# Kernel optimization log

Measured on AMD Instinct MI355X. Metric: run time of the kernel, lower is better.

The kernel has to match this reference:

```python
import jax, jax.numpy as jnp
import numpy as np

B, D, H, T = 256, 1024, 1024, 100
EPS = 1e-5  # torch LayerNorm default

def _ln(x, g, b):
    m = jnp.mean(x, axis=-1, keepdims=True)
    v = jnp.mean((x - m) ** 2, axis=-1, keepdims=True)
    return (x - m) * jax.lax.rsqrt(v + EPS) * g + b

def _gru_cell(x, h, Wih, Whh, bih, bhh):
    # PyTorch GRUCell math. Wih:[3H,in], Whh:[3H,H], gate order r,z,n.
    gi = x @ Wih.T + bih
    gh = h @ Whh.T + bhh
    ir, iz, inn = jnp.split(gi, 3, axis=-1)
    hr, hz, hn = jnp.split(gh, 3, axis=-1)
    r = jax.nn.sigmoid(ir + hr)
    z = jax.nn.sigmoid(iz + hz)
    n = jnp.tanh(inn + r * hn)
    return (1.0 - z) * n + z * h

def setup_inputs() -> dict:
    key = jax.random.key(0)
    ks = jax.random.split(key, 16)
    def xav(k, shape):
        fan_out, fan_in = shape
        lim = np.sqrt(6.0 / (fan_in + fan_out))
        return jax.random.uniform(k, shape, jnp.float32, -lim, lim)
    inp = {
        'x': jax.random.normal(ks[0], (B, D), jnp.float32),
        'enc_W1': xav(ks[1], (H, D)), 'enc_b1': jnp.zeros((H,), jnp.float32),
        'enc_ln1_g': jnp.ones((H,), jnp.float32), 'enc_ln1_b': jnp.zeros((H,), jnp.float32),
        'enc_W2': xav(ks[2], (H, H)), 'enc_b2': jnp.zeros((H,), jnp.float32),
        'enc_ln2_g': jnp.ones((H,), jnp.float32), 'enc_ln2_b': jnp.zeros((H,), jnp.float32),
        'gru_Wih0': jax.random.uniform(ks[3], (3 * H, H), jnp.float32, -1/np.sqrt(H), 1/np.sqrt(H)),
        'gru_Whh0': jax.random.uniform(ks[4], (3 * H, H), jnp.float32, -1/np.sqrt(H), 1/np.sqrt(H)),
        'gru_bih0': jnp.zeros((3 * H,), jnp.float32), 'gru_bhh0': jnp.zeros((3 * H,), jnp.float32),
        'gru_Wih1': jax.random.uniform(ks[5], (3 * H, H), jnp.float32, -1/np.sqrt(H), 1/np.sqrt(H)),
        'gru_Whh1': jax.random.uniform(ks[6], (3 * H, H), jnp.float32, -1/np.sqrt(H), 1/np.sqrt(H)),
        'gru_bih1': jnp.zeros((3 * H,), jnp.float32), 'gru_bhh1': jnp.zeros((3 * H,), jnp.float32),
        'hn_g': jnp.ones((H,), jnp.float32), 'hn_b': jnp.zeros((H,), jnp.float32),
        'proj_W1': xav(ks[7], (H, H)), 'proj_b1': jnp.zeros((H,), jnp.float32),
        'proj_ln_g': jnp.ones((H,), jnp.float32), 'proj_ln_b': jnp.zeros((H,), jnp.float32),
        'proj_W2': xav(ks[8], (D, H)), 'proj_b2': jnp.zeros((D,), jnp.float32),
        'max_length': T,
    }
    return inp

def reference(x, enc_W1, enc_b1, enc_ln1_g, enc_ln1_b, enc_W2, enc_b2, enc_ln2_g, enc_ln2_b,
              gru_Wih0, gru_Whh0, gru_bih0, gru_bhh0, gru_Wih1, gru_Whh1, gru_bih1, gru_bhh1,
              hn_g, hn_b, proj_W1, proj_b1, proj_ln_g, proj_ln_b, proj_W2, proj_b2, max_length):
    # Encoder: Linear -> LN -> ReLU, twice
    e = jax.nn.relu(_ln(x @ enc_W1.T + enc_b1, enc_ln1_g, enc_ln1_b))
    e = jax.nn.relu(_ln(e @ enc_W2.T + enc_b2, enc_ln2_g, enc_ln2_b))
    h_init = jnp.zeros((2, x.shape[0], gru_Whh0.shape[1]), x.dtype)  # [num_layers,B,H]

    def step(carry, _):
        h, cur = carry
        hn = _ln(h, hn_g, hn_b)  # hidden_norm applied to h0 each step
        h0 = _gru_cell(cur, hn[0], gru_Wih0, gru_Whh0, gru_bih0, gru_bhh0)
        h1 = _gru_cell(h0, hn[1], gru_Wih1, gru_Whh1, gru_bih1, gru_bhh1)
        return (jnp.stack([h0, h1]), h1), h1

    (_, _), ys = jax.lax.scan(step, (h_init, e), None, length=max_length)
    outputs = jnp.transpose(ys, (1, 0, 2))  # [B,T,H]
    p = jax.nn.relu(_ln(outputs @ proj_W1.T + proj_b1, proj_ln_g, proj_ln_b))
    return p @ proj_W2.T + proj_b2  # [B,T,D]
```

## Files before the change

### kernel.cpp

```cpp
#include <hip/hip_runtime.h>
#include <stdint.h>

#define T_STEPS 100
#define Bb 256
#define Hh 1024
#define Dd 1024
#define BM 64
#define BN 64
#define BK 64

typedef _Float16 f16;
typedef _Float16 f16x8 __attribute__((ext_vector_type(8)));
typedef _Float16 f16x4 __attribute__((ext_vector_type(4)));
typedef float    f32x4 __attribute__((ext_vector_type(4)));

__global__ __launch_bounds__(256) void k_f32_split(const float* __restrict__ s,
                                                   f16* __restrict__ hi, f16* __restrict__ lo, int n) {
  int i = (blockIdx.x * blockDim.x + threadIdx.x) * 4;
  if (i >= n) return;
  float4 v = *(const float4*)(s + i);
  f16x4 h = { (f16)v.x, (f16)v.y, (f16)v.z, (f16)v.w };
  f16x4 L = { (f16)(v.x - (float)h.x), (f16)(v.y - (float)h.y),
              (f16)(v.z - (float)h.z), (f16)(v.w - (float)h.w) };
  *(f16x4*)(hi + i) = h;
  *(f16x4*)(lo + i) = L;
}

__global__ __launch_bounds__(256) void k_f32_to_f16(const float* __restrict__ s,
                                                    f16* __restrict__ d, int n) {
  int i = (blockIdx.x * blockDim.x + threadIdx.x) * 4;
  if (i >= n) return;
  float4 v = *(const float4*)(s + i);
  f16x4 o = { (f16)v.x, (f16)v.y, (f16)v.z, (f16)v.w };
  *(f16x4*)(d + i) = o;
}

__global__ __launch_bounds__(256) void k_init_hn(const float* __restrict__ lnb,
                                                 float* __restrict__ hn0f, float* __restrict__ hn1f,
                                                 f16* __restrict__ h0hi, f16* __restrict__ h0lo,
                                                 f16* __restrict__ h1hi, f16* __restrict__ h1lo) {
  int m = blockIdx.x, tid = threadIdx.x;
  for (int k = 0; k < 4; ++k) {
    int c = tid + k * 256;
    float v = lnb[c];
    f16 h = (f16)v; f16 L = (f16)(v - (float)h);
    size_t idx = (size_t)m * Hh + c;
    hn0f[idx] = v; hn1f[idx] = v;
    h0hi[idx] = h; h0lo[idx] = L;
    h1hi[idx] = h; h1lo[idx] = L;
  }
}

template <int NCH>
__device__ __forceinline__ void stage_rows(const f16* __restrict__ g, int r0, int k0,
                                           f16* sdst, int tid) {
#pragma unroll
  for (int i = 0; i < NCH; ++i) {
    int slot = i * 256 + tid;
    int row  = slot >> 3;
    int pkg  = slot & 7;
    int lg   = pkg ^ (row & 7);
    const f16* src = g + (size_t)(r0 + row) * 1024 + k0 + lg * 8;
    f16* dst = sdst + (size_t)slot * 8;
    __builtin_amdgcn_global_load_lds((const __attribute__((address_space(1))) void*)src,
                                     (__attribute__((address_space(3))) void*)dst, 16, 0, 0);
  }
}

#define FBM 64
#define FBN 96
__global__ __launch_bounds__(256) void k_gru_gemm(
    const f16* __restrict__ A0h, const f16* __restrict__ A0l,
    const f16* __restrict__ B0h, const f16* __restrict__ B0l, float* __restrict__ C0,
    const f16* __restrict__ A1h, const f16* __restrict__ A1l,
    const f16* __restrict__ B1h, const f16* __restrict__ B1l, float* __restrict__ C1) {
  const int wgid = blockIdx.x;
  const int xcd = wgid & 7, idx = wgid >> 3;
  const int bx = idx & 3, yp = (idx >> 2) & 3, bz = idx >> 4;
  const int by = xcd * 4 + yp;

  const f16* Ah = bz ? A1h : A0h;
  const f16* Al = bz ? A1l : A0l;
  const f16* Bh = bz ? B1h : B0h;
  const f16* Bl = bz ? B1l : B0l;
  float*     C  = bz ? C1  : C0;

  __shared__ alignas(16) f16 sAh[3][FBM * BK];
  __shared__ alignas(16) f16 sAl[3][FBM * BK];
  __shared__ alignas(16) f16 sBh[3][FBN * BK];
  __shared__ alignas(16) f16 sBl[3][FBN * BK];

  const int tid = threadIdx.x;
  const int w = tid >> 6, l = tid & 63;
  const int wr = w >> 1, wc = w & 1;
  const int lrow = l & 15, lkg = l >> 4;
  const int m0 = bx * FBM, n0 = by * FBN;

  f32x4 acc[2][3] = {};

#pragma unroll
  for (int pt = 0; pt < 3; ++pt) {
    stage_rows<2>(Ah, m0, pt * BK, sAh[pt], tid);
    stage_rows<2>(Al, m0, pt * BK, sAl[pt], tid);
    stage_rows<3>(Bh, n0, pt * BK, sBh[pt], tid);
    stage_rows<3>(Bl, n0, pt * BK, sBl[pt], tid);
  }

#pragma unroll
  for (int it = 0; it < 16; ++it) {
    const int cur = it % 3;
    if (it <= 13)      asm volatile("s_waitcnt vmcnt(20)" ::: "memory");
    else if (it == 14) asm volatile("s_waitcnt vmcnt(10)" ::: "memory");
    else               asm volatile("s_waitcnt vmcnt(0)" ::: "memory");
    __builtin_amdgcn_s_barrier();

    f16x8 ah[2][2], al[2][2], bh[2][3], bl[2][3];
#pragma unroll
    for (int ks = 0; ks < 2; ++ks) {
#pragma unroll
      for (int fi = 0; fi < 2; ++fi) {
        int row = wr * 32 + fi * 16 + lrow;
        int pkg = (ks * 4 + lkg) ^ (row & 7);
        ah[ks][fi] = *(const f16x8*)&sAh[cur][row * BK + pkg * 8];
        al[ks][fi] = *(const f16x8*)&sAl[cur][row * BK + pkg * 8];
      }
#pragma unroll
      for (int fj = 0; fj < 3; ++fj) {
        int row = wc * 48 + fj * 16 + lrow;
        int pkg = (ks * 4 + lkg) ^ (row & 7);
        bh[ks][fj] = *(const f16x8*)&sBh[cur][row * BK + pkg * 8];
        bl[ks][fj] = *(const f16x8*)&sBl[cur][row * BK + pkg * 8];
      }
    }
    asm volatile("s_waitcnt lgkmcnt(0)" ::: "memory");
    __builtin_amdgcn_s_barrier();

    if (it < 13) {
      const int k0 = (it + 3) * BK;
      stage_rows<2>(Ah, m0, k0, sAh[cur], tid);
      stage_rows<2>(Al, m0, k0, sAl[cur], tid);
      stage_rows<3>(Bh, n0, k0, sBh[cur], tid);
      stage_rows<3>(Bl, n0, k0, sBl[cur], tid);
    }

#pragma unroll
    for (int ks = 0; ks < 2; ++ks)
#pragma unroll
      for (int fi = 0; fi < 2; ++fi)
#pragma unroll
        for (int fj = 0; fj < 3; ++fj) {
          acc[fi][fj] = __builtin_amdgcn_mfma_f32_16x16x32_f16(ah[ks][fi], bh[ks][fj], acc[fi][fj], 0, 0, 0);
          acc[fi][fj] = __builtin_amdgcn_mfma_f32_16x16x32_f16(ah[ks][fi], bl[ks][fj], acc[fi][fj], 0, 0, 0);
          acc[fi][fj] = __builtin_amdgcn_mfma_f32_16x16x32_f16(al[ks][fi], bh[ks][fj], acc[fi][fj], 0, 0, 0);
        }
  }

#pragma unroll
  for (int fi = 0; fi < 2; ++fi)
#pragma unroll
    for (int fj = 0; fj < 3; ++fj)
#pragma unroll
      for (int r = 0; r < 4; ++r) {
        int row = m0 + wr * 32 + fi * 16 + lkg * 4 + r;
        int col = n0 + wc * 48 + fj * 16 + lrow;
        C[(size_t)row * 3072 + col] = acc[fi][fj][r];
      }
}

__global__ __launch_bounds__(256) void k_gemm_big(const f16* __restrict__ A, const f16* __restrict__ B,
                                                  float* __restrict__ C, const float* __restrict__ bias,
                                                  int N) {
  __shared__ alignas(16) f16 sA[2][128 * BK];
  __shared__ alignas(16) f16 sB[2][128 * BK];
  const int tid = threadIdx.x;
  const int w = tid >> 6, l = tid & 63;
  const int wr = w >> 1, wc = w & 1;
  const int lrow = l & 15, lkg = l >> 4;
  const int m0 = blockIdx.x * 128, n0 = blockIdx.y * 128;

  f32x4 acc[4][4] = {};
  stage_rows<4>(A, m0, 0, sA[0], tid);
  stage_rows<4>(B, n0, 0, sB[0], tid);

  for (int it = 0; it < 16; ++it) {
    __syncthreads();
    const int cur = it & 1;
    if (it < 15) {
      const int k0 = (it + 1) * BK;
      stage_rows<4>(A, m0, k0, sA[cur ^ 1], tid);
      stage_rows<4>(B, n0, k0, sB[cur ^ 1], tid);
    }
#pragma unroll
    for (int ks = 0; ks < 2; ++ks) {
      f16x8 af[4], bf[4];
#pragma unroll
      for (int fi = 0; fi < 4; ++fi) {
        int row = wr * 64 + fi * 16 + lrow;
        int pkg = (ks * 4 + lkg) ^ (row & 7);
        af[fi] = *(const f16x8*)&sA[cur][row * BK + pkg * 8];
      }
#pragma unroll
      for (int fj = 0; fj < 4; ++fj) {
        int row = wc * 64 + fj * 16 + lrow;
        int pkg = (ks * 4 + lkg) ^ (row & 7);
        bf[fj] = *(const f16x8*)&sB[cur][row * BK + pkg * 8];
      }
#pragma unroll
      for (int fi = 0; fi < 4; ++fi)
#pragma unroll
        for (int fj = 0; fj < 4; ++fj)
          acc[fi][fj] = __builtin_amdgcn_mfma_f32_16x16x32_f16(af[fi], bf[fj], acc[fi][fj], 0, 0, 0);
    }
  }
#pragma unroll
  for (int fi = 0; fi < 4; ++fi)
#pragma unroll
    for (int fj = 0; fj < 4; ++fj)
#pragma unroll
      for (int r = 0; r < 4; ++r) {
        int row = m0 + wr * 64 + fi * 16 + lkg * 4 + r;
        int col = n0 + wc * 64 + fj * 16 + lrow;
        C[(size_t)row * N + col] = acc[fi][fj][r] + bias[col];
      }
}

__device__ __forceinline__ void stage_tile(const f16* __restrict__ g, int r0, int k0,
                                           f16* sdst, int tid) {
  stage_rows<2>(g, r0, k0, sdst, tid);
}

__global__ __launch_bounds__(256) void k_gemm3(const f16* __restrict__ Ah, const f16* __restrict__ Al,
                                               const f16* __restrict__ Bh, const f16* __restrict__ Bl,
                                               float* __restrict__ C, const float* __restrict__ bias,
                                               int N) {
  __shared__ alignas(16) f16 sA[2][BM * BK];
  __shared__ alignas(16) f16 sB[2][BN * BK];
  const int tid = threadIdx.x;
  const int w = tid >> 6, l = tid & 63;
  const int wr = w >> 1, wc = w & 1;
  const int lrow = l & 15, lkg = l >> 4;
  const int m0 = blockIdx.x * BM, n0 = blockIdx.y * BN;
  const int TOT = 48;

  f32x4 acc[2][2] = {};
  stage_tile(Ah, m0, 0, sA[0], tid);
  stage_tile(Bh, n0, 0, sB[0], tid);

  for (int it = 0; it < TOT; ++it) {
    __syncthreads();
    const int cur = it & 1;
    if (it + 1 < TOT) {
      const int nx = it + 1;
      const f16* An = (nx >= 32) ? Al : Ah;
      const f16* Bn = ((nx >> 4) == 1) ? Bl : Bh;
      const int k0 = (nx & 15) * BK;
      stage_tile(An, m0, k0, sA[cur ^ 1], tid);
      stage_tile(Bn, n0, k0, sB[cur ^ 1], tid);
    }
#pragma unroll
    for (int ks = 0; ks < 2; ++ks) {
      f16x8 af[2], bf[2];
#pragma unroll
      for (int fi = 0; fi < 2; ++fi) {
        int row = wr * 32 + fi * 16 + lrow;
        int pkg = (ks * 4 + lkg) ^ (row & 7);
        af[fi] = *(const f16x8*)&sA[cur][row * BK + pkg * 8];
      }
#pragma unroll
      for (int fj = 0; fj < 2; ++fj) {
        int row = wc * 32 + fj * 16 + lrow;
        int pkg = (ks * 4 + lkg) ^ (row & 7);
        bf[fj] = *(const f16x8*)&sB[cur][row * BK + pkg * 8];
      }
#pragma unroll
      for (int fi = 0; fi < 2; ++fi)
#pragma unroll
        for (int fj = 0; fj < 2; ++fj)
          acc[fi][fj] = __builtin_amdgcn_mfma_f32_16x16x32_f16(af[fi], bf[fj], acc[fi][fj], 0, 0, 0);
    }
  }
#pragma unroll
  for (int fi = 0; fi < 2; ++fi)
#pragma unroll
    for (int fj = 0; fj < 2; ++fj)
#pragma unroll
      for (int r = 0; r < 4; ++r) {
        int row = m0 + wr * 32 + fi * 16 + lkg * 4 + r;
        int col = n0 + wc * 32 + fj * 16 + lrow;
        C[(size_t)row * N + col] = acc[fi][fj][r] + (bias ? bias[col] : 0.f);
      }
}

__device__ __forceinline__ void block_sum2(float& a, float& b) {
#pragma unroll
  for (int o = 32; o > 0; o >>= 1) { a += __shfl_down(a, o, 64); b += __shfl_down(b, o, 64); }
  __shared__ float sa[4], sb[4];
  int w = threadIdx.x >> 6, l = threadIdx.x & 63;
  if (l == 0) { sa[w] = a; sb[w] = b; }
  __syncthreads();
  a = sa[0] + sa[1] + sa[2] + sa[3];
  b = sb[0] + sb[1] + sb[2] + sb[3];
}

__device__ __forceinline__ void split_store(float v, f16* hi, f16* lo, size_t idx) {
  f16 h = (f16)v;
  hi[idx] = h;
  lo[idx] = (f16)(v - (float)h);
}

__global__ __launch_bounds__(256) void k_gru_gate(const float* __restrict__ gi, const float* __restrict__ gh,
                                                  float* __restrict__ hnf,
                                                  f16* __restrict__ hnhi, f16* __restrict__ hnlo,
                                                  f16* __restrict__ xhi, f16* __restrict__ xlo,
                                                  const float* __restrict__ bih, const float* __restrict__ bhh,
                                                  const float* __restrict__ lng, const float* __restrict__ lnb,
                                                  f16* __restrict__ outp, long ostride) {
  int m = blockIdx.x, tid = threadIdx.x;
  float h[4];
  float s1 = 0.f, s2 = 0.f;
#pragma unroll
  for (int k = 0; k < 4; ++k) {
    int c = tid + k * 256;
    size_t g0 = (size_t)m * (3 * Hh) + c;
    float rr  = (gi[g0]          + bih[c])          + (gh[g0]          + bhh[c]);
    float zz  = (gi[g0 + Hh]     + bih[Hh + c])     + (gh[g0 + Hh]     + bhh[Hh + c]);
    float in_ =  gi[g0 + 2 * Hh] + bih[2 * Hh + c];
    float hn_ =  gh[g0 + 2 * Hh] + bhh[2 * Hh + c];
    float r = 1.f / (1.f + expf(-rr));
    float z = 1.f / (1.f + expf(-zz));
    float n = tanhf(in_ + r * hn_);
    float hp = hnf[(size_t)m * Hh + c];
    float hv = (1.f - z) * n + z * hp;
    h[k] = hv;
    split_store(hv, xhi, xlo, (size_t)m * Hh + c);
    if (outp) outp[(size_t)m * ostride + c] = (f16)hv;
    s1 += hv; s2 += hv * hv;
  }
  block_sum2(s1, s2);
  float mean = s1 * (1.f / Hh);
  float var  = s2 * (1.f / Hh) - mean * mean;
  float rs   = rsqrtf(var + 1e-5f);
#pragma unroll
  for (int k = 0; k < 4; ++k) {
    int c = tid + k * 256;
    float v = (h[k] - mean) * rs * lng[c] + lnb[c];
    hnf[(size_t)m * Hh + c] = v;
    split_store(v, hnhi, hnlo, (size_t)m * Hh + c);
  }
}

__global__ __launch_bounds__(256) void k_ln_relu(const float* __restrict__ pre,
                                                 const float* __restrict__ g, const float* __restrict__ b,
                                                 f16* __restrict__ hi, f16* __restrict__ lo) {
  int m = blockIdx.x, tid = threadIdx.x;
  float v[4]; float s1 = 0.f, s2 = 0.f;
#pragma unroll
  for (int k = 0; k < 4; ++k) {
    int c = tid + k * 256;
    float x = pre[(size_t)m * Hh + c];
    v[k] = x; s1 += x; s2 += x * x;
  }
  block_sum2(s1, s2);
  float mean = s1 * (1.f / Hh);
  float var  = s2 * (1.f / Hh) - mean * mean;
  float rs   = rsqrtf(var + 1e-5f);
#pragma unroll
  for (int k = 0; k < 4; ++k) {
    int c = tid + k * 256;
    float y = (v[k] - mean) * rs * g[c] + b[c];
    y = y > 0.f ? y : 0.f;
    f16 hh = (f16)y;
    hi[(size_t)m * Hh + c] = hh;
    if (lo) lo[(size_t)m * Hh + c] = (f16)(y - (float)hh);
  }
}

extern "C" void kernel_launch(void* const* d_in, const int* in_sizes, int n_in,
                              void* d_out, int out_size, void* d_ws, size_t ws_size,
                              hipStream_t stream) {
  (void)in_sizes; (void)n_in; (void)out_size; (void)ws_size;
  const float* x     = (const float*)d_in[0];
  const float* encW1 = (const float*)d_in[1];
  const float* encb1 = (const float*)d_in[2];
  const float* ln1g  = (const float*)d_in[3];
  const float* ln1b  = (const float*)d_in[4];
  const float* encW2 = (const float*)d_in[5];
  const float* encb2 = (const float*)d_in[6];
  const float* ln2g  = (const float*)d_in[7];
  const float* ln2b  = (const float*)d_in[8];
  const float* Wih0  = (const float*)d_in[9];
  const float* Whh0  = (const float*)d_in[10];
  const float* bih0  = (const float*)d_in[11];
  const float* bhh0  = (const float*)d_in[12];
  const float* Wih1  = (const float*)d_in[13];
  const float* Whh1  = (const float*)d_in[14];
  const float* bih1  = (const float*)d_in[15];
  const float* bhh1  = (const float*)d_in[16];
  const float* hng   = (const float*)d_in[17];
  const float* hnb   = (const float*)d_in[18];
  const float* pW1   = (const float*)d_in[19];
  const float* pb1   = (const float*)d_in[20];
  const float* plng  = (const float*)d_in[21];
  const float* plnb  = (const float*)d_in[22];
  const float* pW2   = (const float*)d_in[23];
  const float* pb2   = (const float*)d_in[24];

  char* p = (char*)d_ws;
  auto alloc = [&](size_t bytes) { void* r = (void*)p; p += (bytes + 255) & ~(size_t)255; return r; };
  auto fpair = [&](size_t n, f16** hi, f16** lo) {
    *hi = (f16*)alloc(n * 2); *lo = (f16*)alloc(n * 2);
  };
  f16 *We1h, *We1l, *We2h, *We2l, *Wih0h, *Wih0l, *Whh0h, *Whh0l, *Wih1h, *Wih1l, *Whh1h, *Whh1l;
  fpair((size_t)Hh * Dd, &We1h, &We1l);
  fpair((size_t)Hh * Hh, &We2h, &We2l);
  fpair((size_t)3 * Hh * Hh, &Wih0h, &Wih0l);
  fpair((size_t)3 * Hh * Hh, &Whh0h, &Whh0l);
  fpair((size_t)3 * Hh * Hh, &Wih1h, &Wih1l);
  fpair((size_t)3 * Hh * Hh, &Whh1h, &Whh1l);
  f16* pW1h = (f16*)alloc((size_t)Hh * Hh * 2);
  f16* pW2h = (f16*)alloc((size_t)Dd * Hh * 2);
  f16 *xhi, *xlo, *curh, *curl, *x1h, *x1l, *hn0h, *hn0l, *hn1h, *hn1l;
  fpair((size_t)Bb * Dd, &xhi, &xlo);
  fpair((size_t)Bb * Hh, &curh, &curl);
  fpair((size_t)Bb * Hh, &x1h, &x1l);
  fpair((size_t)Bb * Hh, &hn0h, &hn0l);
  fpair((size_t)Bb * Hh, &hn1h, &hn1l);
  float* hn0f = (float*)alloc((size_t)Bb * Hh * 4);
  float* hn1f = (float*)alloc((size_t)Bb * Hh * 4);
  float* gif  = (float*)alloc((size_t)Bb * 3 * Hh * 4);
  float* ghf  = (float*)alloc((size_t)Bb * 3 * Hh * 4);
  f16* outsh  = (f16*)alloc((size_t)Bb * T_STEPS * Hh * 2);
  f16* ph     = outsh;
  float* pre  = (float*)d_out;

  auto spl = [&](const float* s, f16* hi, f16* lo, int n) {
    hipLaunchKernelGGL(k_f32_split, dim3((n / 4 + 255) / 256), dim3(256), 0, stream, s, hi, lo, n);
  };
  auto conv = [&](const float* s, f16* d, int n) {
    hipLaunchKernelGGL(k_f32_to_f16, dim3((n / 4 + 255) / 256), dim3(256), 0, stream, s, d, n);
  };
  spl(x, xhi, xlo, Bb * Dd);
  spl(encW1, We1h, We1l, Hh * Dd);
  spl(encW2, We2h, We2l, Hh * Hh);
  spl(Wih0, Wih0h, Wih0l, 3 * Hh * Hh);
  spl(Whh0, Whh0h, Whh0l, 3 * Hh * Hh);
  spl(Wih1, Wih1h, Wih1l, 3 * Hh * Hh);
  spl(Whh1, Whh1h, Whh1l, 3 * Hh * Hh);
  conv(pW1, pW1h, Hh * Hh);
  conv(pW2, pW2h, Dd * Hh);
  hipLaunchKernelGGL(k_init_hn, dim3(Bb), dim3(256), 0, stream, hnb, hn0f, hn1f, hn0h, hn0l, hn1h, hn1l);

  hipLaunchKernelGGL(k_gemm3, dim3(Bb / BM, Hh / BN), dim3(256), 0, stream,
                     xhi, xlo, We1h, We1l, gif, encb1, Hh);
  hipLaunchKernelGGL(k_ln_relu, dim3(Bb), dim3(256), 0, stream, gif, ln1g, ln1b, x1h, x1l);
  hipLaunchKernelGGL(k_gemm3, dim3(Bb / BM, Hh / BN), dim3(256), 0, stream,
                     x1h, x1l, We2h, We2l, gif, encb2, Hh);
  hipLaunchKernelGGL(k_ln_relu, dim3(Bb), dim3(256), 0, stream, gif, ln2g, ln2b, curh, curl);

  for (int t = 0; t < T_STEPS; ++t) {
    hipLaunchKernelGGL(k_gru_gemm, dim3(256), dim3(256), 0, stream,
                       curh, curl, Wih0h, Wih0l, gif, hn0h, hn0l, Whh0h, Whh0l, ghf);
    hipLaunchKernelGGL(k_gru_gate, dim3(Bb), dim3(256), 0, stream,
                       gif, ghf, hn0f, hn0h, hn0l, x1h, x1l, bih0, bhh0, hng, hnb,
                       (f16*)nullptr, (long)0);
    hipLaunchKernelGGL(k_gru_gemm, dim3(256), dim3(256), 0, stream,
                       x1h, x1l, Wih1h, Wih1l, gif, hn1h, hn1l, Whh1h, Whh1l, ghf);
    hipLaunchKernelGGL(k_gru_gate, dim3(Bb), dim3(256), 0, stream,
                       gif, ghf, hn1f, hn1h, hn1l, curh, curl, bih1, bhh1, hng, hnb,
                       outsh + (size_t)t * Hh, (long)T_STEPS * Hh);
  }

  hipLaunchKernelGGL(k_gemm_big, dim3(Bb * T_STEPS / 128, Hh / 128), dim3(256), 0, stream,
                     outsh, pW1h, pre, pb1, Hh);
  hipLaunchKernelGGL(k_ln_relu, dim3(Bb * T_STEPS), dim3(256), 0, stream, pre, plng, plnb,
                     ph, (f16*)nullptr);
  hipLaunchKernelGGL(k_gemm_big, dim3(Bb * T_STEPS / 128, Dd / 128), dim3(256), 0, stream,
                     ph, pW2h, (float*)d_out, pb2, Dd);
}
```

Baseline: 4.692 ms.

## Load GRU GEMM fragments directly from global memory, dropping LDS pipeline

The recurrent GRU GEMM kernel no longer stages A/B hi/lo tiles through a triple-buffered LDS pipeline with barriers. Each lane now reads its MFMA fragments straight from global memory via per-lane row pointers. Launch bounds now request one block per SM. This removes LDS staging, waitcnt, and barrier overhead on a small per-step GEMM, but loses cross-wave reuse of loaded tiles. It therefore relies on L1/L2 caching, and the scattered 16-byte loads may be less coalesced.

```diff
diff --git a/kernel.cpp b/kernel.cpp
--- a/kernel.cpp
+++ b/kernel.cpp
@@ -51,12 +51,12 @@
   }
 }
 
-template <int NCH>
+template <int NCH, int NT>
 __device__ __forceinline__ void stage_rows(const f16* __restrict__ g, int r0, int k0,
                                            f16* sdst, int tid) {
 #pragma unroll
   for (int i = 0; i < NCH; ++i) {
-    int slot = i * 256 + tid;
+    int slot = i * NT + tid;
     int row  = slot >> 3;
     int pkg  = slot & 7;
     int lg   = pkg ^ (row & 7);
@@ -69,7 +69,7 @@
 
 #define FBM 64
 #define FBN 96
-__global__ __launch_bounds__(256) void k_gru_gemm(
+__global__ __launch_bounds__(256, 1) void k_gru_gemm(
     const f16* __restrict__ A0h, const f16* __restrict__ A0l,
     const f16* __restrict__ B0h, const f16* __restrict__ B0l, float* __restrict__ C0,
     const f16* __restrict__ A1h, const f16* __restrict__ A1l,
@@ -85,64 +85,36 @@
   const f16* Bl = bz ? B1l : B0l;
   float*     C  = bz ? C1  : C0;
 
-  __shared__ alignas(16) f16 sAh[3][FBM * BK];
-  __shared__ alignas(16) f16 sAl[3][FBM * BK];
-  __shared__ alignas(16) f16 sBh[3][FBN * BK];
-  __shared__ alignas(16) f16 sBl[3][FBN * BK];
-
   const int tid = threadIdx.x;
   const int w = tid >> 6, l = tid & 63;
   const int wr = w >> 1, wc = w & 1;
   const int lrow = l & 15, lkg = l >> 4;
   const int m0 = bx * FBM, n0 = by * FBN;
 
+  const f16* pa_h = Ah + (size_t)(m0 + wr * 32 + lrow) * 1024 + lkg * 8;
+  const f16* pa_l = Al + (size_t)(m0 + wr * 32 + lrow) * 1024 + lkg * 8;
+  const f16* pb_h = Bh + (size_t)(n0 + wc * 48 + lrow) * 1024 + lkg * 8;
+  const f16* pb_l = Bl + (size_t)(n0 + wc * 48 + lrow) * 1024 + lkg * 8;
+
   f32x4 acc[2][3] = {};
 
 #pragma unroll
-  for (int pt = 0; pt < 3; ++pt) {
-    stage_rows<2>(Ah, m0, pt * BK, sAh[pt], tid);
-    stage_rows<2>(Al, m0, pt * BK, sAl[pt], tid);
-    stage_rows<3>(Bh, n0, pt * BK, sBh[pt], tid);
-    stage_rows<3>(Bl, n0, pt * BK, sBl[pt], tid);
-  }
-
-#pragma unroll
-  for (int it = 0; it < 16; ++it) {
-    const int cur = it % 3;
-    if (it <= 13)      asm volatile("s_waitcnt vmcnt(20)" ::: "memory");
-    else if (it == 14) asm volatile("s_waitcnt vmcnt(10)" ::: "memory");
-    else               asm volatile("s_waitcnt vmcnt(0)" ::: "memory");
-    __builtin_amdgcn_s_barrier();
-
+  for (int j = 0; j < 16; ++j) {
     f16x8 ah[2][2], al[2][2], bh[2][3], bl[2][3];
 #pragma unroll
     for (int ks = 0; ks < 2; ++ks) {
+      const int ko = j * 64 + ks * 32;
 #pragma unroll
       for (int fi = 0; fi < 2; ++fi) {
-        int row = wr * 32 + fi * 16 + lrow;
-        int pkg = (ks * 4 + lkg) ^ (row & 7);
-        ah[ks][fi] = *(const f16x8*)&sAh[cur][row * BK + pkg * 8];
-        al[ks][fi] = *(const f16x8*)&sAl[cur][row * BK + pkg * 8];
+        ah[ks][fi] = *(const f16x8*)(pa_h + (size_t)fi * 16 * 1024 + ko);
+        al[ks][fi] = *(const f16x8*)(pa_l + (size_t)fi * 16 * 1024 + ko);
       }
 #pragma unroll
       for (int fj = 0; fj < 3; ++fj) {
-        int row = wc * 48 + fj * 16 + lrow;
-        int pkg = (ks * 4 + lkg) ^ (row & 7);
-        bh[ks][fj] = *(const f16x8*)&sBh[cur][row * BK + pkg * 8];
-        bl[ks][fj] = *(const f16x8*)&sBl[cur][row * BK + pkg * 8];
+        bh[ks][fj] = *(const f16x8*)(pb_h + (size_t)fj * 16 * 1024 + ko);
+        bl[ks][fj] = *(const f16x8*)(pb_l + (size_t)fj * 16 * 1024 + ko);
       }
     }
-    asm volatile("s_waitcnt lgkmcnt(0)" ::: "memory");
-    __builtin_amdgcn_s_barrier();
-
-    if (it < 13) {
-      const int k0 = (it + 3) * BK;
-      stage_rows<2>(Ah, m0, k0, sAh[cur], tid);
-      stage_rows<2>(Al, m0, k0, sAl[cur], tid);
-      stage_rows<3>(Bh, n0, k0, sBh[cur], tid);
-      stage_rows<3>(Bl, n0, k0, sBl[cur], tid);
-    }
-
 #pragma unroll
     for (int ks = 0; ks < 2; ++ks)
 #pragma unroll
@@ -179,16 +151,16 @@
   const int m0 = blockIdx.x * 128, n0 = blockIdx.y * 128;
 
   f32x4 acc[4][4] = {};
-  stage_rows<4>(A, m0, 0, sA[0], tid);
-  stage_rows<4>(B, n0, 0, sB[0], tid);
+  stage_rows<4, 256>(A, m0, 0, sA[0], tid);
+  stage_rows<4, 256>(B, n0, 0, sB[0], tid);
 
   for (int it = 0; it < 16; ++it) {
     __syncthreads();
     const int cur = it & 1;
     if (it < 15) {
       const int k0 = (it + 1) * BK;
-      stage_rows<4>(A, m0, k0, sA[cur ^ 1], tid);
-      stage_rows<4>(B, n0, k0, sB[cur ^ 1], tid);
+      stage_rows<4, 256>(A, m0, k0, sA[cur ^ 1], tid);
+      stage_rows<4, 256>(B, n0, k0, sB[cur ^ 1], tid);
     }
 #pragma unroll
     for (int ks = 0; ks < 2; ++ks) {
@@ -226,7 +198,7 @@
 
 __device__ __forceinline__ void stage_tile(const f16* __restrict__ g, int r0, int k0,
                                            f16* sdst, int tid) {
-  stage_rows<2>(g, r0, k0, sdst, tid);
+  stage_rows<2, 256>(g, r0, k0, sdst, tid);
 }
 
 __global__ __launch_bounds__(256) void k_gemm3(const f16* __restrict__ Ah, const f16* __restrict__ Al,
```

Measured after the change: 9.687 ms. +106.5%, slower.
